# Performance work log

Hardware: AMD Instinct MI355X
Metric: run time of the kernel (lower is better)

## Reference

```python
import jax, jax.numpy as jnp
import numpy as np

B = 131072  # batch of chess positions


def _window_idx():
    # For window i: x=i//6, y=i%6; gather 3x3 squares, 6 features each -> 54 cols
    idx = np.zeros((36, 54), dtype=np.int32)
    for i in range(36):
        x, y = i // 6, i % 6
        cols = []
        for ox in range(3):
            for oy in range(3):
                base = (x + ox) * 8 * 6 + (y + oy) * 6
                cols.extend(range(base, base + 6))
        idx[i] = cols
    return jnp.asarray(idx)

_IDX = _window_idx()  # [36, 54]


def crelu(x):
    return jnp.clip(x, -1.0, 1.0)


def setup_inputs() -> dict:
    key = jax.random.key(0)
    ks = jax.random.split(key, 13)
    s = 0.3  # weight scale
    return {
        "inp": jax.random.normal(ks[0], (B, 385), dtype=jnp.float32),
        "W1": jax.random.normal(ks[1], (54, 12), dtype=jnp.float32) * s,
        "b1": jax.random.normal(ks[2], (12,), dtype=jnp.float32) * s,
        "W2": jax.random.normal(ks[3], (12, 12), dtype=jnp.float32) * s,
        "b2": jax.random.normal(ks[4], (12,), dtype=jnp.float32) * s,
        "W3": jax.random.normal(ks[5], (12, 4), dtype=jnp.float32) * s,
        "b3": jax.random.normal(ks[6], (4,), dtype=jnp.float32) * s,
        "V1": jax.random.normal(ks[7], (145, 32), dtype=jnp.float32) * s,
        "c1": jax.random.normal(ks[8], (32,), dtype=jnp.float32) * s,
        "V2": jax.random.normal(ks[9], (32, 32), dtype=jnp.float32) * s,
        "c2": jax.random.normal(ks[10], (32,), dtype=jnp.float32) * s,
        "V3": jax.random.normal(ks[11], (32, 1), dtype=jnp.float32) * s,
        "c3": jax.random.normal(ks[12], (1,), dtype=jnp.float32) * s,
    }


def reference(inp, W1, b1, W2, b2, W3, b3, V1, c1, V2, c2, V3, c3):
    b = inp.shape[0]
    win = inp[:, _IDX]                               # [B, 36, 54] im2col gather
    h = crelu(jnp.einsum("bwk,kn->bwn", win, W1) + b1)   # [B, 36, 12]
    h = crelu(h @ W2 + b2)                           # [B, 36, 12]
    sight = crelu(h @ W3 + b3)                       # [B, 36, 4]
    vision = jnp.concatenate([sight.reshape(b, 144), inp[:, 384:385]], axis=1)  # [B,145]
    e = crelu(vision @ V1 + c1)                      # [B, 32]
    e = crelu(e @ V2 + c2)                           # [B, 32]
    return crelu(e @ V3 + c3)                        # [B, 1]
```

## Files before the change

kernel.cpp:

```cpp
#include <hip/hip_runtime.h>
#include <hip/hip_bf16.h>

#define NT   384
#define SPB  32
#define LSTR 386
#define LPAD 64

typedef __attribute__((ext_vector_type(4))) float     f32x4;
typedef __attribute__((ext_vector_type(8))) _Float16  f16x8;
typedef __attribute__((ext_vector_type(4))) _Float16  f16x4;

union U8 { f16x8 v; unsigned u[4]; };
union U4 { f16x4 v; unsigned u[2]; };

static __device__ inline unsigned pack_f16(float a, float b) {
    union { _Float16 h[2]; unsigned u; } c;
    c.h[0] = (_Float16)a; c.h[1] = (_Float16)b;
    return c.u;
}
static __device__ inline void split_pack(float a, float b, unsigned& hi, unsigned& lo) {
    const _Float16 ah = (_Float16)a, bh = (_Float16)b;
    hi = pack_f16((float)ah, (float)bh);
    lo = pack_f16(a - (float)ah, b - (float)bh);
}
static __device__ inline unsigned short to_f16u(float a) {
    union { _Float16 h; unsigned short u; } c;
    c.h = (_Float16)a;
    return c.u;
}
static __device__ inline float clamp1(float v) { return fminf(fmaxf(v, -1.f), 1.f); }

static __device__ inline f32x4 mfma32(f16x8 a, f16x8 b, f32x4 c) {
    return __builtin_amdgcn_mfma_f32_16x16x32_f16(a, b, c, 0, 0, 0);
}
static __device__ inline f32x4 mfma16(f16x4 a, f16x4 b, f32x4 c) {
#if __has_builtin(__builtin_amdgcn_mfma_f32_16x16x16f16)
    return __builtin_amdgcn_mfma_f32_16x16x16f16(a, b, c, 0, 0, 0);
#else
    f32x4 d;
    asm volatile("v_mfma_f32_16x16x16_f16 %0, %1, %2, %3\n\ts_nop 7\n\ts_nop 1"
                 : "=v"(d) : "v"(a), "v"(b), "v"(c));
    return d;
#endif
}

__global__ __launch_bounds__(NT, 4)
void lila_fused(const float* __restrict__ inp,
                const float* __restrict__ W1, const float* __restrict__ b1,
                const float* __restrict__ W2, const float* __restrict__ b2,
                const float* __restrict__ W3, const float* __restrict__ b3,
                const float* __restrict__ V1, const float* __restrict__ c1,
                const float* __restrict__ V2, const float* __restrict__ c2,
                const float* __restrict__ V3, const float* __restrict__ c3,
                float* __restrict__ out)
{
    __shared__ __align__(16) unsigned short lbuf16[SPB * LSTR + LPAD];
    __shared__ __align__(16) float lsight[SPB * 148];
    __shared__ __align__(16) float le1[SPB * 33];

    const int tid  = threadIdx.x;
    const int lid  = tid & 63;
    const int wv   = tid >> 6;
    const int quad = lid >> 4;
    const int c16  = lid & 15;
    const int s0   = blockIdx.x * SPB;

    U8 wa1h[2], wa1l[2];
    #pragma unroll
    for (int f = 0; f < 2; ++f)
        #pragma unroll
        for (int j2 = 0; j2 < 4; ++j2) {
            const int k0 = f * 32 + quad * 8 + 2 * j2;
            const float v0 = (k0     < 54 && c16 < 12) ? W1[k0 * 12 + c16]       : 0.f;
            const float v1 = (k0 + 1 < 54 && c16 < 12) ? W1[(k0 + 1) * 12 + c16] : 0.f;
            split_pack(v0, v1, wa1h[f].u[j2], wa1l[f].u[j2]);
        }
    U4 wa2h, wa2l, wa3h, wa3l;
    #pragma unroll
    for (int j2 = 0; j2 < 2; ++j2) {
        const int k0 = quad * 4 + 2 * j2;
        const float a0 = (k0     < 12 && c16 < 12) ? W2[k0 * 12 + c16]       : 0.f;
        const float a1 = (k0 + 1 < 12 && c16 < 12) ? W2[(k0 + 1) * 12 + c16] : 0.f;
        split_pack(a0, a1, wa2h.u[j2], wa2l.u[j2]);
        const float g0 = (k0     < 12 && c16 < 4) ? W3[k0 * 4 + c16]       : 0.f;
        const float g1 = (k0 + 1 < 12 && c16 < 4) ? W3[(k0 + 1) * 4 + c16] : 0.f;
        split_pack(g0, g1, wa3h.u[j2], wa3l.u[j2]);
    }
    float b1v[4], b2v[4], b3v[4];
    #pragma unroll
    for (int r = 0; r < 4; ++r) {
        const int c = quad * 4 + r;
        b1v[r] = (c < 12) ? b1[c] : 0.f;
        b2v[r] = (c < 12) ? b2[c] : 0.f;
        b3v[r] = (c < 4)  ? b3[c] : 0.f;
    }
    int dofs[8]; unsigned msk[8];
    #pragma unroll
    for (int p = 0; p < 8; ++p) {
        const int k = (p >> 2) * 32 + quad * 8 + 2 * (p & 3);
        dofs[p] = (k / 18) * 48 + (k % 18);
        msk[p]  = (k < 54) ? 0xFFFFFFFFu : 0u;
    }

    {
        const float* g = inp + (size_t)s0 * 385;
        #pragma unroll 4
        for (int r = 0; r < SPB; ++r)
            lbuf16[r * LSTR + tid] = to_f16u(g[r * 385 + tid]);
    }
    __syncthreads();

    const f32x4 z = {0.f, 0.f, 0.f, 0.f};
    for (int t = wv; t < (SPB * 36) / 16; t += NT / 64) {
        const int r = t * 16 + c16;
        const int s = r / 36;
        const int w = r - s * 36;
        const int x = w / 6;
        const int y = w - x * 6;
        const int base = s * LSTR + x * 48 + y * 6;

        U8 bw[2];
        #pragma unroll
        for (int p = 0; p < 8; ++p) {
            unsigned v = *(const unsigned*)(&lbuf16[base + dofs[p]]);
            bw[p >> 2].u[p & 3] = v & msk[p];
        }

        f32x4 acc = z;
        acc = mfma32(wa1h[0].v, bw[0].v, acc);
        acc = mfma32(wa1h[1].v, bw[1].v, acc);
        acc = mfma32(wa1l[0].v, bw[0].v, acc);
        acc = mfma32(wa1l[1].v, bw[1].v, acc);

        U4 bb2;
        bb2.u[0] = pack_f16(clamp1(acc[0] + b1v[0]), clamp1(acc[1] + b1v[1]));
        bb2.u[1] = pack_f16(clamp1(acc[2] + b1v[2]), clamp1(acc[3] + b1v[3]));
        f32x4 d2 = mfma16(wa2h.v, bb2.v, z);
        d2 = mfma16(wa2l.v, bb2.v, d2);

        U4 bb3;
        bb3.u[0] = pack_f16(clamp1(d2[0] + b2v[0]), clamp1(d2[1] + b2v[1]));
        bb3.u[1] = pack_f16(clamp1(d2[2] + b2v[2]), clamp1(d2[3] + b2v[3]));
        f32x4 d3 = mfma16(wa3h.v, bb3.v, z);
        d3 = mfma16(wa3l.v, bb3.v, d3);

        if (lid < 16) {
            f32x4 q = { clamp1(d3[0] + b3v[0]), clamp1(d3[1] + b3v[1]),
                        clamp1(d3[2] + b3v[2]), clamp1(d3[3] + b3v[3]) };
            *(f32x4*)&lsight[s * 148 + w * 4] = q;
        }
    }
    __syncthreads();

    {
        float4*       dst = (float4*)lbuf16;
        const float4* v1g = (const float4*)V1;
        for (int i = tid; i < (145 * 32) / 4; i += NT) dst[i] = v1g[i];
        const float4* v2g = (const float4*)V2;
        for (int i = tid; i < (32 * 32) / 4; i += NT) dst[(145 * 32) / 4 + i] = v2g[i];
    }
    __syncthreads();

    const float* lv1 = (const float*)lbuf16;
    const float* lw2 = lv1 + 145 * 32;

    if (tid < 8 * SPB) {
        const int s  = tid >> 3;
        const int c0 = (tid & 7) * 4;
        const float lastv = inp[(size_t)(s0 + s) * 385 + 384];

        float4 e = *(const float4*)(c1 + c0);
        const float* sgp = lsight + s * 148;
        #pragma unroll 4
        for (int r4 = 0; r4 < 36; ++r4) {
            const float4 sv = *(const float4*)(sgp + r4 * 4);
            const float svv[4] = {sv.x, sv.y, sv.z, sv.w};
            #pragma unroll
            for (int j = 0; j < 4; ++j) {
                const float v = svv[j];
                const float4 wv4 = *(const float4*)(lv1 + (r4 * 4 + j) * 32 + c0);
                e.x = fmaf(v, wv4.x, e.x);
                e.y = fmaf(v, wv4.y, e.y);
                e.z = fmaf(v, wv4.z, e.z);
                e.w = fmaf(v, wv4.w, e.w);
            }
        }
        {
            const float4 wv4 = *(const float4*)(lv1 + 144 * 32 + c0);
            e.x = fmaf(lastv, wv4.x, e.x);
            e.y = fmaf(lastv, wv4.y, e.y);
            e.z = fmaf(lastv, wv4.z, e.z);
            e.w = fmaf(lastv, wv4.w, e.w);
        }
        le1[s * 33 + c0 + 0] = clamp1(e.x);
        le1[s * 33 + c0 + 1] = clamp1(e.y);
        le1[s * 33 + c0 + 2] = clamp1(e.z);
        le1[s * 33 + c0 + 3] = clamp1(e.w);
    }
    __syncthreads();

    if (tid < 8 * SPB) {
        const int s  = tid >> 3;
        const int c0 = (tid & 7) * 4;

        float4 f = *(const float4*)(c2 + c0);
        #pragma unroll
        for (int r = 0; r < 32; ++r) {
            const float v = le1[s * 33 + r];
            const float4 wv4 = *(const float4*)(lw2 + r * 32 + c0);
            f.x = fmaf(v, wv4.x, f.x);
            f.y = fmaf(v, wv4.y, f.y);
            f.z = fmaf(v, wv4.z, f.z);
            f.w = fmaf(v, wv4.w, f.w);
        }
        f.x = clamp1(f.x);
        f.y = clamp1(f.y);
        f.z = clamp1(f.z);
        f.w = clamp1(f.w);

        const float4 v3 = *(const float4*)(V3 + c0);
        float part = f.x * v3.x + f.y * v3.y + f.z * v3.z + f.w * v3.w;
        part += __shfl_xor(part, 1);
        part += __shfl_xor(part, 2);
        part += __shfl_xor(part, 4);
        if ((tid & 7) == 0)
            out[s0 + s] = clamp1(part + c3[0]);
    }
}

extern "C" void kernel_launch(void* const* d_in, const int* in_sizes, int n_in,
                              void* d_out, int out_size, void* d_ws, size_t ws_size,
                              hipStream_t stream) {
    const float* inp = (const float*)d_in[0];
    const float* W1  = (const float*)d_in[1];
    const float* b1  = (const float*)d_in[2];
    const float* W2  = (const float*)d_in[3];
    const float* b2  = (const float*)d_in[4];
    const float* W3  = (const float*)d_in[5];
    const float* b3  = (const float*)d_in[6];
    const float* V1  = (const float*)d_in[7];
    const float* c1  = (const float*)d_in[8];
    const float* V2  = (const float*)d_in[9];
    const float* c2  = (const float*)d_in[10];
    const float* V3  = (const float*)d_in[11];
    const float* c3  = (const float*)d_in[12];
    float* out = (float*)d_out;

    const int Btot   = in_sizes[0] / 385;
    const int blocks = Btot / SPB;

    lila_fused<<<dim3(blocks), dim3(NT), 0, stream>>>(
        inp, W1, b1, W2, b2, W3, b3, V1, c1, V2, c2, V3, c3, out);
}
```

Before: 360.8 us.

## Move head MLP layers to split-f16 MFMA with prepacked weights, halve samples per block

Replaces the scalar FP32 FMA loops for the V1 and V2 head layers with MFMA 16x16x32 f16 ops, using a hi/lo split of each operand to keep accuracy close to fp32. A small pre-kernel packs V1/V2 into hi/lo f16 pairs in the workspace on every call, so blocks no longer copy the weights into LDS. Sight outputs are written directly as packed split pairs into a swizzled LDS layout. SPB drops to 16 and launch bounds rise to 6 blocks per CU, trading per-block work for occupancy at the cost of an extra launch and global weight reads per block.

```diff
diff --git a/kernel.cpp b/kernel.cpp
--- a/kernel.cpp
+++ b/kernel.cpp
@@ -1,10 +1,12 @@
 #include <hip/hip_runtime.h>
-#include <hip/hip_bf16.h>
 
 #define NT   384
-#define SPB  32
+#define SPB  16
 #define LSTR 386
 #define LPAD 64
+
+#define WS_V2_OFF 2560
+#define WS_SLOTS  3072
 
 typedef __attribute__((ext_vector_type(4))) float     f32x4;
 typedef __attribute__((ext_vector_type(8))) _Float16  f16x8;
@@ -44,19 +46,40 @@
 #endif
 }
 
-__global__ __launch_bounds__(NT, 4)
+__global__ void lila_pack(const float* __restrict__ V1h, const float* __restrict__ V2h,
+                          uint2* __restrict__ ws)
+{
+    const int i = blockIdx.x * 256 + threadIdx.x;
+    if (i >= WS_SLOTS) return;
+    float a, b;
+    if (i < WS_V2_OFF) {
+        const int p = i >> 5, n = i & 31;
+        a = (2 * p     < 145) ? V1h[(2 * p)     * 32 + n] : 0.f;
+        b = (2 * p + 1 < 145) ? V1h[(2 * p + 1) * 32 + n] : 0.f;
+    } else {
+        const int j = i - WS_V2_OFF;
+        const int p = j >> 5, n = j & 31;
+        a = V2h[(2 * p)     * 32 + n];
+        b = V2h[(2 * p + 1) * 32 + n];
+    }
+    uint2 t;
+    split_pack(a, b, t.x, t.y);
+    ws[i] = t;
+}
+
+__global__ __launch_bounds__(NT, 6)
 void lila_fused(const float* __restrict__ inp,
                 const float* __restrict__ W1, const float* __restrict__ b1,
                 const float* __restrict__ W2, const float* __restrict__ b2,
                 const float* __restrict__ W3, const float* __restrict__ b3,
-                const float* __restrict__ V1, const float* __restrict__ c1,
-                const float* __restrict__ V2, const float* __restrict__ c2,
+                const float* __restrict__ c1, const float* __restrict__ c2,
                 const float* __restrict__ V3, const float* __restrict__ c3,
+                const uint2* __restrict__ wpk,
                 float* __restrict__ out)
 {
     __shared__ __align__(16) unsigned short lbuf16[SPB * LSTR + LPAD];
-    __shared__ __align__(16) float lsight[SPB * 148];
-    __shared__ __align__(16) float le1[SPB * 33];
+    __shared__ __align__(16) uint2 vis[80 * 16];
+    __shared__ __align__(16) uint2 le1u[16 * 16];
 
     const int tid  = threadIdx.x;
     const int lid  = tid & 63;
@@ -107,6 +130,16 @@
         #pragma unroll 4
         for (int r = 0; r < SPB; ++r)
             lbuf16[r * LSTR + tid] = to_f16u(g[r * 385 + tid]);
+        if (tid < 128) {
+            const int p = 72 + (tid >> 4);
+            const int s = tid & 15;
+            uint2 t; t.x = 0u; t.y = 0u;
+            if (p == 72) {
+                const float lv = g[s * 385 + 384];
+                split_pack(lv, 0.f, t.x, t.y);
+            }
+            vis[p * 16 + ((s + p) & 15)] = t;
+        }
     }
     __syncthreads();
 
@@ -145,86 +178,84 @@
         d3 = mfma16(wa3l.v, bb3.v, d3);
 
         if (lid < 16) {
-            f32x4 q = { clamp1(d3[0] + b3v[0]), clamp1(d3[1] + b3v[1]),
-                        clamp1(d3[2] + b3v[2]), clamp1(d3[3] + b3v[3]) };
-            *(f32x4*)&lsight[s * 148 + w * 4] = q;
+            const float v0 = clamp1(d3[0] + b3v[0]);
+            const float v1 = clamp1(d3[1] + b3v[1]);
+            const float v2 = clamp1(d3[2] + b3v[2]);
+            const float v3 = clamp1(d3[3] + b3v[3]);
+            unsigned h01, l01, h23, l23;
+            split_pack(v0, v1, h01, l01);
+            split_pack(v2, v3, h23, l23);
+            const int p0 = 2 * w;
+            uint2 t0; t0.x = h01; t0.y = l01;
+            uint2 t1; t1.x = h23; t1.y = l23;
+            vis[p0       * 16 + ((s + p0)     & 15)] = t0;
+            vis[(p0 + 1) * 16 + ((s + p0 + 1) & 15)] = t1;
         }
     }
     __syncthreads();
 
-    {
-        float4*       dst = (float4*)lbuf16;
-        const float4* v1g = (const float4*)V1;
-        for (int i = tid; i < (145 * 32) / 4; i += NT) dst[i] = v1g[i];
-        const float4* v2g = (const float4*)V2;
-        for (int i = tid; i < (32 * 32) / 4; i += NT) dst[(145 * 32) / 4 + i] = v2g[i];
+    if (wv < 2) {
+        const int nt = wv;
+        f32x4 acc = z;
+        #pragma unroll
+        for (int kk = 0; kk < 5; ++kk) {
+            U8 ah, al, bh, bl;
+            #pragma unroll
+            for (int j2 = 0; j2 < 4; ++j2) {
+                const int p = kk * 16 + quad * 4 + j2;
+                const uint2 a = wpk[p * 32 + nt * 16 + c16];
+                ah.u[j2] = a.x; al.u[j2] = a.y;
+                const uint2 b = vis[p * 16 + ((c16 + p) & 15)];
+                bh.u[j2] = b.x; bl.u[j2] = b.y;
+            }
+            acc = mfma32(al.v, bl.v, acc);
+            acc = mfma32(al.v, bh.v, acc);
+            acc = mfma32(ah.v, bl.v, acc);
+            acc = mfma32(ah.v, bh.v, acc);
+        }
+        const float4 c1v = *(const float4*)(c1 + nt * 16 + quad * 4);
+        const float e0 = clamp1(acc[0] + c1v.x);
+        const float e1 = clamp1(acc[1] + c1v.y);
+        const float e2 = clamp1(acc[2] + c1v.z);
+        const float e3 = clamp1(acc[3] + c1v.w);
+        unsigned h01, l01, h23, l23;
+        split_pack(e0, e1, h01, l01);
+        split_pack(e2, e3, h23, l23);
+        const int p0 = nt * 8 + quad * 2;
+        uint2 t0; t0.x = h01; t0.y = l01;
+        uint2 t1; t1.x = h23; t1.y = l23;
+        le1u[p0       * 16 + ((c16 + p0)     & 15)] = t0;
+        le1u[(p0 + 1) * 16 + ((c16 + p0 + 1) & 15)] = t1;
     }
     __syncthreads();
 
-    const float* lv1 = (const float*)lbuf16;
-    const float* lw2 = lv1 + 145 * 32;
-
-    if (tid < 8 * SPB) {
-        const int s  = tid >> 3;
-        const int c0 = (tid & 7) * 4;
-        const float lastv = inp[(size_t)(s0 + s) * 385 + 384];
-
-        float4 e = *(const float4*)(c1 + c0);
-        const float* sgp = lsight + s * 148;
-        #pragma unroll 4
-        for (int r4 = 0; r4 < 36; ++r4) {
-            const float4 sv = *(const float4*)(sgp + r4 * 4);
-            const float svv[4] = {sv.x, sv.y, sv.z, sv.w};
+    if (wv == 0) {
+        float part = 0.f;
+        #pragma unroll
+        for (int nt2 = 0; nt2 < 2; ++nt2) {
+            U8 ah, al, bh, bl;
             #pragma unroll
-            for (int j = 0; j < 4; ++j) {
-                const float v = svv[j];
-                const float4 wv4 = *(const float4*)(lv1 + (r4 * 4 + j) * 32 + c0);
-                e.x = fmaf(v, wv4.x, e.x);
-                e.y = fmaf(v, wv4.y, e.y);
-                e.z = fmaf(v, wv4.z, e.z);
-                e.w = fmaf(v, wv4.w, e.w);
+            for (int j2 = 0; j2 < 4; ++j2) {
+                const int p = quad * 4 + j2;
+                const uint2 a = wpk[WS_V2_OFF + p * 32 + nt2 * 16 + c16];
+                ah.u[j2] = a.x; al.u[j2] = a.y;
+                const uint2 b = le1u[p * 16 + ((c16 + p) & 15)];
+                bh.u[j2] = b.x; bl.u[j2] = b.y;
             }
-        }
-        {
-            const float4 wv4 = *(const float4*)(lv1 + 144 * 32 + c0);
-            e.x = fmaf(lastv, wv4.x, e.x);
-            e.y = fmaf(lastv, wv4.y, e.y);
-            e.z = fmaf(lastv, wv4.z, e.z);
-            e.w = fmaf(lastv, wv4.w, e.w);
-        }
-        le1[s * 33 + c0 + 0] = clamp1(e.x);
-        le1[s * 33 + c0 + 1] = clamp1(e.y);
-        le1[s * 33 + c0 + 2] = clamp1(e.z);
-        le1[s * 33 + c0 + 3] = clamp1(e.w);
-    }
-    __syncthreads();
-
-    if (tid < 8 * SPB) {
-        const int s  = tid >> 3;
-        const int c0 = (tid & 7) * 4;
-
-        float4 f = *(const float4*)(c2 + c0);
-        #pragma unroll
-        for (int r = 0; r < 32; ++r) {
-            const float v = le1[s * 33 + r];
-            const float4 wv4 = *(const float4*)(lw2 + r * 32 + c0);
-            f.x = fmaf(v, wv4.x, f.x);
-            f.y = fmaf(v, wv4.y, f.y);
-            f.z = fmaf(v, wv4.z, f.z);
-            f.w = fmaf(v, wv4.w, f.w);
-        }
-        f.x = clamp1(f.x);
-        f.y = clamp1(f.y);
-        f.z = clamp1(f.z);
-        f.w = clamp1(f.w);
-
-        const float4 v3 = *(const float4*)(V3 + c0);
-        float part = f.x * v3.x + f.y * v3.y + f.z * v3.z + f.w * v3.w;
-        part += __shfl_xor(part, 1);
-        part += __shfl_xor(part, 2);
-        part += __shfl_xor(part, 4);
-        if ((tid & 7) == 0)
-            out[s0 + s] = clamp1(part + c3[0]);
+            f32x4 d = z;
+            d = mfma32(al.v, bl.v, d);
+            d = mfma32(al.v, bh.v, d);
+            d = mfma32(ah.v, bl.v, d);
+            d = mfma32(ah.v, bh.v, d);
+            const float4 c2v = *(const float4*)(c2 + nt2 * 16 + quad * 4);
+            const float4 v3v = *(const float4*)(V3 + nt2 * 16 + quad * 4);
+            part += clamp1(d[0] + c2v.x) * v3v.x + clamp1(d[1] + c2v.y) * v3v.y
+                  + clamp1(d[2] + c2v.z) * v3v.z + clamp1(d[3] + c2v.w) * v3v.w;
+        }
+        part += __shfl_xor(part, 16);
+        part += __shfl_xor(part, 32);
+        if (lid < 16)
+            out[s0 + c16] = clamp1(part + c3[0]);
     }
 }
 
@@ -246,9 +277,12 @@
     const float* c3  = (const float*)d_in[12];
     float* out = (float*)d_out;
 
+    uint2* wpk = (uint2*)d_ws;
+    lila_pack<<<dim3((WS_SLOTS + 255) / 256), dim3(256), 0, stream>>>(V1, V2, wpk);
+
     const int Btot   = in_sizes[0] / 385;
     const int blocks = Btot / SPB;
 
     lila_fused<<<dim3(blocks), dim3(NT), 0, stream>>>(
-        inp, W1, b1, W2, b2, W3, b3, V1, c1, V2, c2, V3, c3, out);
-}
+        inp, W1, b1, W2, b2, W3, b3, c1, c2, V3, c3, wpk, out);
+}
```

Measured after the change: 401.0 us. +11.1%, slower.
